# Kernel optimization log

Measured on AMD Instinct MI355X. Metric: run time of the kernel, lower is better.

The kernel has to match this reference:

```python
import jax, jax.numpy as jnp
import numpy as np

TOP_K = 8
ROUTE_SCALE = 2.5
NUM_EXPERTS = 64


def setup_inputs() -> dict:
    key = jax.random.key(0)
    k1, k2, k3 = jax.random.split(key, 3)
    x = jax.random.normal(k1, (16384, 4096), dtype=jnp.float32)
    gate_weight = jax.random.normal(k2, (NUM_EXPERTS, 4096), dtype=jnp.float32) * 0.02
    expert_bias = jax.random.normal(k3, (NUM_EXPERTS,), dtype=jnp.float32) * 0.01
    return {"x": x, "gate_weight": gate_weight, "expert_bias": expert_bias}


def reference(x, gate_weight, expert_bias):
    # gate linear: [T, dim] @ [dim, E] -> [T, E]
    logits = jnp.einsum("td,ed->te", x, gate_weight)
    scores = jax.nn.sigmoid(logits.astype(jnp.float32))  # score_func == 'sigmoid'
    # expert_bias branch: top-k over biased scores, gather unbiased scores
    _, selected_experts_indices = jax.lax.top_k(scores + expert_bias[None, :], TOP_K)
    top_scores = jnp.take_along_axis(scores, selected_experts_indices, axis=1)
    # route_norm (sigmoid normalization)
    denom = top_scores.sum(axis=-1, keepdims=True) + 1e-20
    top_scores = top_scores / denom * ROUTE_SCALE
    # histogram over selected expert indices (torch.histc returns float)
    flat_idx = selected_experts_indices.reshape(-1)
    num_tokens_per_expert = jnp.zeros((NUM_EXPERTS,), jnp.float32).at[flat_idx].add(1.0)
    return top_scores, selected_experts_indices, num_tokens_per_expert
```

## Files before the change

kernel.cpp:

```cpp
#include <hip/hip_runtime.h>
#include <math.h>

#define NTOK 16384
#define DIM  4096
#define NE   64
#define TOPK 8
#define SPLITK 8
#define NSLICE (DIM / SPLITK / 32)
#define ROUTE_SCALE 2.5f

typedef __attribute__((ext_vector_type(8))) short short8v;
typedef __attribute__((ext_vector_type(4))) float f32x4;

__device__ __forceinline__ void split3_pack(const float* v, uint4& b0, uint4& b1, uint4& b2)
{
    uint p0[8], p1[8], p2[8];
#pragma unroll
    for (int j = 0; j < 8; ++j) {
        const float xv = v[j];
        const uint  u0 = __float_as_uint(xv) & 0xffff0000u;
        const float f0 = __uint_as_float(u0);
        const float r  = xv - f0;
        const uint  u1 = __float_as_uint(r) & 0xffff0000u;
        const float f1 = __uint_as_float(u1);
        const float r2 = r - f1;
        const uint  u2 = __float_as_uint(r2) & 0xffff0000u;
        p0[j] = u0; p1[j] = u1; p2[j] = u2;
    }
    b0 = make_uint4(p0[1] | (p0[0] >> 16), p0[3] | (p0[2] >> 16),
                    p0[5] | (p0[4] >> 16), p0[7] | (p0[6] >> 16));
    b1 = make_uint4(p1[1] | (p1[0] >> 16), p1[3] | (p1[2] >> 16),
                    p1[5] | (p1[4] >> 16), p1[7] | (p1[6] >> 16));
    b2 = make_uint4(p2[1] | (p2[0] >> 16), p2[3] | (p2[2] >> 16),
                    p2[5] | (p2[4] >> 16), p2[7] | (p2[6] >> 16));
}

__global__ __launch_bounds__(256)
void prep_w(const float* __restrict__ gw, uint4* __restrict__ wS)
{
    const int tid  = blockIdx.x * 256 + threadIdx.x;
    const int lane = tid & 63;
    const int nt   = (tid >> 6) & 3;
    const int ks   = tid >> 8;
    const int e    = nt * 16 + (lane & 15);
    const int kb   = ks * 32 + (lane >> 4) * 8;
    float v[8];
    *(float4*)&v[0] = *(const float4*)&gw[(size_t)e * DIM + kb];
    *(float4*)&v[4] = *(const float4*)&gw[(size_t)e * DIM + kb + 4];
    uint4 b0, b1, b2;
    split3_pack(v, b0, b1, b2);
    const size_t base = (size_t)(ks * 4 + nt) * 3 * 64 + lane;
    wS[base] = b0; wS[base + 64] = b1; wS[base + 128] = b2;
}

__global__ __launch_bounds__(512, 2)
void router_fused(const float* __restrict__ x, const uint4* __restrict__ wS,
                  const float* __restrict__ bias, float* __restrict__ out)
{
    __shared__ float part_lds[SPLITK][64][NE];
    __shared__ int   hist[NE];

    const int t    = threadIdx.x;
    const int lane = t & 63;
    const int wv   = __builtin_amdgcn_readfirstlane(t >> 6);
    const int r    = lane & 15;
    const int g    = lane >> 4;
    const int tok0 = blockIdx.x * 64;
    const int ks0  = wv * NSLICE;

    if (t < NE) hist[t] = 0;

    const float* xr[4];
#pragma unroll
    for (int G = 0; G < 4; ++G)
        xr[G] = x + (size_t)(tok0 + G * 16 + r) * DIM + ks0 * 32 + g * 8;
    const uint4* wB = wS + lane;

    f32x4 acc[16];
#pragma unroll
    for (int i = 0; i < 16; ++i) acc[i] = (f32x4){0.f, 0.f, 0.f, 0.f};

    float xP[32], xQ[32];
    uint4 bP[12], bQ[12];

#define LOADX(X, s) do {                                                     \
        _Pragma("unroll")                                                    \
        for (int G = 0; G < 4; ++G) {                                        \
            *(float4*)&X[G * 8]     = *(const float4*)(xr[G] + (size_t)(s) * 32);     \
            *(float4*)&X[G * 8 + 4] = *(const float4*)(xr[G] + (size_t)(s) * 32 + 4); \
        }                                                                    \
    } while (0)
#define LOADB(B, s) do {                                                     \
        _Pragma("unroll")                                                    \
        for (int i = 0; i < 12; ++i)                                         \
            B[i] = wB[((size_t)(ks0 + (s)) * 12 + i) * 64];                  \
    } while (0)
#define COMPUTE(X, B) do {                                                            \
        _Pragma("unroll")                                                             \
        for (int G = 0; G < 4; ++G) {                                                 \
            uint4 a0u, a1u, a2u;                                                      \
            split3_pack(&X[G * 8], a0u, a1u, a2u);                                    \
            const short8v a0 = *(short8v*)&a0u;                                       \
            const short8v a1 = *(short8v*)&a1u;                                       \
            const short8v a2 = *(short8v*)&a2u;                                       \
            _Pragma("unroll")                                                         \
            for (int nt = 0; nt < 4; ++nt) {                                          \
                const short8v b0 = *(const short8v*)&B[nt * 3 + 0];                   \
                const short8v b1 = *(const short8v*)&B[nt * 3 + 1];                   \
                const short8v b2 = *(const short8v*)&B[nt * 3 + 2];                   \
                f32x4 c = acc[nt * 4 + G];                                            \
                c = __builtin_amdgcn_mfma_f32_16x16x32_bf16(a2, b0, c, 0, 0, 0);      \
                c = __builtin_amdgcn_mfma_f32_16x16x32_bf16(a1, b1, c, 0, 0, 0);      \
                c = __builtin_amdgcn_mfma_f32_16x16x32_bf16(a0, b2, c, 0, 0, 0);      \
                c = __builtin_amdgcn_mfma_f32_16x16x32_bf16(a1, b0, c, 0, 0, 0);      \
                c = __builtin_amdgcn_mfma_f32_16x16x32_bf16(a0, b1, c, 0, 0, 0);      \
                c = __builtin_amdgcn_mfma_f32_16x16x32_bf16(a0, b0, c, 0, 0, 0);      \
                acc[nt * 4 + G] = c;                                                  \
            }                                                                         \
        }                                                                             \
    } while (0)

    LOADX(xP, 0);
    for (int it = 0; it < NSLICE / 2; ++it) {
        const int s = 2 * it;
        LOADB(bP, s);
        LOADX(xQ, s + 1);
        COMPUTE(xP, bP);
        LOADB(bQ, s + 1);
        const int s2 = (s + 2) & (NSLICE - 1);
        LOADX(xP, s2);
        COMPUTE(xQ, bQ);
    }
#undef LOADX
#undef LOADB
#undef COMPUTE

#pragma unroll
    for (int nt = 0; nt < 4; ++nt)
#pragma unroll
        for (int G = 0; G < 4; ++G)
#pragma unroll
            for (int q = 0; q < 4; ++q)
                part_lds[wv][G * 16 + g * 4 + q][nt * 16 + r] = acc[nt * 4 + G][q];

    __syncthreads();

    const float bias_l = bias[lane];
#pragma unroll 1
    for (int i = 0; i < 8; ++i) {
        const int tok = wv * 8 + i;
        float logit = 0.f;
#pragma unroll
        for (int kh = 0; kh < SPLITK; ++kh)
            logit += part_lds[kh][tok][lane];
        const float s = 1.f / (1.f + expf(-logit));
        float myv  = s + bias_l;
        float outv = 0.f;
        int   outi = 0;
        float sum  = 0.f;
#pragma unroll
        for (int k = 0; k < TOPK; ++k) {
            float cv = myv;
            int   ci = lane;
#pragma unroll
            for (int off = 32; off; off >>= 1) {
                float ov = __shfl_xor(cv, off, 64);
                int   oi = __shfl_xor(ci, off, 64);
                if (ov > cv || (ov == cv && oi < ci)) { cv = ov; ci = oi; }
            }
            float ts = __shfl(s, ci, 64);
            sum += ts;
            if (lane == k)  { outv = ts; outi = ci; }
            if (lane == ci) { myv = -1e30f; }
        }
        const float denom = sum + 1e-20f;
        const size_t gt = (size_t)tok0 + tok;
        if (lane < TOPK) {
            out[gt * TOPK + lane] = (outv / denom) * ROUTE_SCALE;
            out[(size_t)NTOK * TOPK + gt * TOPK + lane] = (float)outi;
            atomicAdd(&hist[outi], 1);
        }
    }

    __syncthreads();
    if (t < NE) {
        int c = hist[t];
        if (c) atomicAdd(&out[(size_t)NTOK * TOPK * 2 + t], (float)c);
    }
}

extern "C" void kernel_launch(void* const* d_in, const int* in_sizes, int n_in,
                              void* d_out, int out_size, void* d_ws, size_t ws_size,
                              hipStream_t stream)
{
    const float* x    = (const float*)d_in[0];
    const float* gw   = (const float*)d_in[1];
    const float* bias = (const float*)d_in[2];
    float* out = (float*)d_out;
    uint4* wS  = (uint4*)d_ws;

    hipMemsetAsync(out + (size_t)NTOK * TOPK * 2, 0, NE * sizeof(float), stream);

    prep_w<<<128, 256, 0, stream>>>(gw, wS);
    router_fused<<<NTOK / 64, 512, 0, stream>>>(x, wS, bias, out);
}
```

Measured before the change: 116.2 us.

## Stage x chunks through swizzled LDS and split waves by token/expert instead of split-K

```diff
diff --git a/kernel.cpp b/kernel.cpp
--- a/kernel.cpp
+++ b/kernel.cpp
@@ -5,8 +5,9 @@
 #define DIM  4096
 #define NE   64
 #define TOPK 8
-#define SPLITK 8
-#define NSLICE (DIM / SPLITK / 32)
+#define CHUNK 256
+#define NCH  (DIM / CHUNK)
+#define SLC  (CHUNK / 32)
 #define ROUTE_SCALE 2.5f
 
 typedef __attribute__((ext_vector_type(8))) short short8v;
@@ -57,103 +58,105 @@
 void router_fused(const float* __restrict__ x, const uint4* __restrict__ wS,
                   const float* __restrict__ bias, float* __restrict__ out)
 {
-    __shared__ float part_lds[SPLITK][64][NE];
+    __shared__ float xs[2][64][CHUNK];
+    __shared__ float sc[64][NE + 1];
     __shared__ int   hist[NE];
 
     const int t    = threadIdx.x;
     const int lane = t & 63;
     const int wv   = __builtin_amdgcn_readfirstlane(t >> 6);
-    const int r    = lane & 15;
+    const int r15  = lane & 15;
     const int g    = lane >> 4;
+    const int tg   = wv & 3;
+    const int eh   = wv >> 2;
     const int tok0 = blockIdx.x * 64;
-    const int ks0  = wv * NSLICE;
 
     if (t < NE) hist[t] = 0;
 
-    const float* xr[4];
-#pragma unroll
-    for (int G = 0; G < 4; ++G)
-        xr[G] = x + (size_t)(tok0 + G * 16 + r) * DIM + ks0 * 32 + g * 8;
-    const uint4* wB = wS + lane;
-
-    f32x4 acc[16];
-#pragma unroll
-    for (int i = 0; i < 16; ++i) acc[i] = (f32x4){0.f, 0.f, 0.f, 0.f};
-
-    float xP[32], xQ[32];
-    uint4 bP[12], bQ[12];
-
-#define LOADX(X, s) do {                                                     \
-        _Pragma("unroll")                                                    \
-        for (int G = 0; G < 4; ++G) {                                        \
-            *(float4*)&X[G * 8]     = *(const float4*)(xr[G] + (size_t)(s) * 32);     \
-            *(float4*)&X[G * 8 + 4] = *(const float4*)(xr[G] + (size_t)(s) * 32 + 4); \
-        }                                                                    \
-    } while (0)
-#define LOADB(B, s) do {                                                     \
-        _Pragma("unroll")                                                    \
-        for (int i = 0; i < 12; ++i)                                         \
-            B[i] = wB[((size_t)(ks0 + (s)) * 12 + i) * 64];                  \
-    } while (0)
-#define COMPUTE(X, B) do {                                                            \
-        _Pragma("unroll")                                                             \
-        for (int G = 0; G < 4; ++G) {                                                 \
-            uint4 a0u, a1u, a2u;                                                      \
-            split3_pack(&X[G * 8], a0u, a1u, a2u);                                    \
-            const short8v a0 = *(short8v*)&a0u;                                       \
-            const short8v a1 = *(short8v*)&a1u;                                       \
-            const short8v a2 = *(short8v*)&a2u;                                       \
-            _Pragma("unroll")                                                         \
-            for (int nt = 0; nt < 4; ++nt) {                                          \
-                const short8v b0 = *(const short8v*)&B[nt * 3 + 0];                   \
-                const short8v b1 = *(const short8v*)&B[nt * 3 + 1];                   \
-                const short8v b2 = *(const short8v*)&B[nt * 3 + 2];                   \
-                f32x4 c = acc[nt * 4 + G];                                            \
-                c = __builtin_amdgcn_mfma_f32_16x16x32_bf16(a2, b0, c, 0, 0, 0);      \
-                c = __builtin_amdgcn_mfma_f32_16x16x32_bf16(a1, b1, c, 0, 0, 0);      \
-                c = __builtin_amdgcn_mfma_f32_16x16x32_bf16(a0, b2, c, 0, 0, 0);      \
-                c = __builtin_amdgcn_mfma_f32_16x16x32_bf16(a1, b0, c, 0, 0, 0);      \
-                c = __builtin_amdgcn_mfma_f32_16x16x32_bf16(a0, b1, c, 0, 0, 0);      \
-                c = __builtin_amdgcn_mfma_f32_16x16x32_bf16(a0, b0, c, 0, 0, 0);      \
-                acc[nt * 4 + G] = c;                                                  \
-            }                                                                         \
-        }                                                                             \
-    } while (0)
-
-    LOADX(xP, 0);
-    for (int it = 0; it < NSLICE / 2; ++it) {
-        const int s = 2 * it;
-        LOADB(bP, s);
-        LOADX(xQ, s + 1);
-        COMPUTE(xP, bP);
-        LOADB(bQ, s + 1);
-        const int s2 = (s + 2) & (NSLICE - 1);
-        LOADX(xP, s2);
-        COMPUTE(xQ, bQ);
-    }
-#undef LOADX
-#undef LOADB
-#undef COMPUTE
-
-#pragma unroll
-    for (int nt = 0; nt < 4; ++nt)
-#pragma unroll
-        for (int G = 0; G < 4; ++G)
-#pragma unroll
-            for (int q = 0; q < 4; ++q)
-                part_lds[wv][G * 16 + g * 4 + q][nt * 16 + r] = acc[nt * 4 + G][q];
-
+    const int row = tg * 16 + r15;
+    const int sw  = r15 & 7;
+    const float* xstage = x + (size_t)(tok0 + wv * 8) * DIM + lane * 4;
+    const uint4* wB = wS + (size_t)(eh * 6) * 64 + lane;
+
+    f32x4 acc[2];
+    acc[0] = (f32x4){0.f, 0.f, 0.f, 0.f};
+    acc[1] = (f32x4){0.f, 0.f, 0.f, 0.f};
+
+    float4 st[8];
+    uint4  b[4][6];
+
+#pragma unroll
+    for (int i = 0; i < 8; ++i)
+        st[i] = *(const float4*)(xstage + (size_t)i * DIM);
+#pragma unroll
+    for (int i = 0; i < 8; ++i)
+        *(float4*)&xs[0][wv * 8 + i][(lane ^ i) * 4] = st[i];
+
+    for (int c = 0; c < NCH; ++c) {
+        const int  cb   = c & 1;
+        const bool more = (c + 1 < NCH);
+        __syncthreads();
+#pragma unroll
+        for (int s = 0; s < 4; ++s)
+#pragma unroll
+            for (int j = 0; j < 6; ++j)
+                b[s][j] = wB[((size_t)(c * SLC + s) * 12 + j) * 64];
+        if (more) {
+#pragma unroll
+            for (int i = 0; i < 8; ++i)
+                st[i] = *(const float4*)(xstage + (size_t)i * DIM + (size_t)(c + 1) * CHUNK);
+        }
+#pragma unroll
+        for (int s = 0; s < SLC; ++s) {
+            float a8[8];
+            const int G0 = s * 8 + g * 2;
+            *(float4*)&a8[0] = *(const float4*)&xs[cb][row][(G0 ^ sw) * 4];
+            *(float4*)&a8[4] = *(const float4*)&xs[cb][row][((G0 + 1) ^ sw) * 4];
+            uint4 a0u, a1u, a2u;
+            split3_pack(a8, a0u, a1u, a2u);
+            const short8v a0 = *(short8v*)&a0u;
+            const short8v a1 = *(short8v*)&a1u;
+            const short8v a2 = *(short8v*)&a2u;
+#pragma unroll
+            for (int ntl = 0; ntl < 2; ++ntl) {
+                const short8v b0 = *(const short8v*)&b[s & 3][ntl * 3 + 0];
+                const short8v b1 = *(const short8v*)&b[s & 3][ntl * 3 + 1];
+                const short8v b2 = *(const short8v*)&b[s & 3][ntl * 3 + 2];
+                f32x4 cc = acc[ntl];
+                cc = __builtin_amdgcn_mfma_f32_16x16x32_bf16(a2, b0, cc, 0, 0, 0);
+                cc = __builtin_amdgcn_mfma_f32_16x16x32_bf16(a1, b1, cc, 0, 0, 0);
+                cc = __builtin_amdgcn_mfma_f32_16x16x32_bf16(a0, b2, cc, 0, 0, 0);
+                cc = __builtin_amdgcn_mfma_f32_16x16x32_bf16(a1, b0, cc, 0, 0, 0);
+                cc = __builtin_amdgcn_mfma_f32_16x16x32_bf16(a0, b1, cc, 0, 0, 0);
+                cc = __builtin_amdgcn_mfma_f32_16x16x32_bf16(a0, b0, cc, 0, 0, 0);
+                acc[ntl] = cc;
+            }
+            if (s < 4) {
+#pragma unroll
+                for (int j = 0; j < 6; ++j)
+                    b[s & 3][j] = wB[((size_t)(c * SLC + s + 4) * 12 + j) * 64];
+            }
+            if (s == 5 && more) {
+#pragma unroll
+                for (int i = 0; i < 8; ++i)
+                    *(float4*)&xs[cb ^ 1][wv * 8 + i][(lane ^ i) * 4] = st[i];
+            }
+        }
+    }
+
+#pragma unroll
+    for (int ntl = 0; ntl < 2; ++ntl)
+#pragma unroll
+        for (int q = 0; q < 4; ++q)
+            sc[tg * 16 + g * 4 + q][eh * 32 + ntl * 16 + r15] =
+                1.f / (1.f + expf(-acc[ntl][q]));
     __syncthreads();
 
     const float bias_l = bias[lane];
 #pragma unroll 1
     for (int i = 0; i < 8; ++i) {
         const int tok = wv * 8 + i;
-        float logit = 0.f;
-#pragma unroll
-        for (int kh = 0; kh < SPLITK; ++kh)
-            logit += part_lds[kh][tok][lane];
-        const float s = 1.f / (1.f + expf(-logit));
+        const float s = sc[tok][lane];
         float myv  = s + bias_l;
         float outv = 0.f;
         int   outi = 0;
@@ -184,8 +187,8 @@
 
     __syncthreads();
     if (t < NE) {
-        int c = hist[t];
-        if (c) atomicAdd(&out[(size_t)NTOK * TOPK * 2 + t], (float)c);
+        int cgt = hist[t];
+        if (cgt) atomicAdd(&out[(size_t)NTOK * TOPK * 2 + t], (float)cgt);
     }
 }
 
```

After: 205.0 us. 1.76x slower.

## Split experts across waves with LDS-staged pre-split x chunks instead of split-K

Applied to the files above, without the earlier changes.

```diff
diff --git a/kernel.cpp b/kernel.cpp
--- a/kernel.cpp
+++ b/kernel.cpp
@@ -5,8 +5,9 @@
 #define DIM  4096
 #define NE   64
 #define TOPK 8
-#define SPLITK 8
-#define NSLICE (DIM / SPLITK / 32)
+#define TPB  32
+#define CHUNK 128
+#define NCH  (DIM / CHUNK)
 #define ROUTE_SCALE 2.5f
 
 typedef __attribute__((ext_vector_type(8))) short short8v;
@@ -33,6 +34,27 @@
                     p1[5] | (p1[4] >> 16), p1[7] | (p1[6] >> 16));
     b2 = make_uint4(p2[1] | (p2[0] >> 16), p2[3] | (p2[2] >> 16),
                     p2[5] | (p2[4] >> 16), p2[7] | (p2[6] >> 16));
+}
+
+__device__ __forceinline__ void split3_pack4(const float4 v, uint2& q0, uint2& q1, uint2& q2)
+{
+    const float vv[4] = {v.x, v.y, v.z, v.w};
+    uint p0[4], p1[4], p2[4];
+#pragma unroll
+    for (int j = 0; j < 4; ++j) {
+        const float xv = vv[j];
+        const uint  u0 = __float_as_uint(xv) & 0xffff0000u;
+        const float f0 = __uint_as_float(u0);
+        const float r  = xv - f0;
+        const uint  u1 = __float_as_uint(r) & 0xffff0000u;
+        const float f1 = __uint_as_float(u1);
+        const float r2 = r - f1;
+        const uint  u2 = __float_as_uint(r2) & 0xffff0000u;
+        p0[j] = u0; p1[j] = u1; p2[j] = u2;
+    }
+    q0 = make_uint2(p0[1] | (p0[0] >> 16), p0[3] | (p0[2] >> 16));
+    q1 = make_uint2(p1[1] | (p1[0] >> 16), p1[3] | (p1[2] >> 16));
+    q2 = make_uint2(p2[1] | (p2[0] >> 16), p2[3] | (p2[2] >> 16));
 }
 
 __global__ __launch_bounds__(256)
@@ -53,107 +75,122 @@
     wS[base] = b0; wS[base + 64] = b1; wS[base + 128] = b2;
 }
 
-__global__ __launch_bounds__(512, 2)
+#define MFMA6(A0, A1, A2, B0, B1, B2, ACC) do {                              \
+    ACC = __builtin_amdgcn_mfma_f32_16x16x32_bf16(A2, B0, ACC, 0, 0, 0);     \
+    ACC = __builtin_amdgcn_mfma_f32_16x16x32_bf16(A1, B1, ACC, 0, 0, 0);     \
+    ACC = __builtin_amdgcn_mfma_f32_16x16x32_bf16(A0, B2, ACC, 0, 0, 0);     \
+    ACC = __builtin_amdgcn_mfma_f32_16x16x32_bf16(A1, B0, ACC, 0, 0, 0);     \
+    ACC = __builtin_amdgcn_mfma_f32_16x16x32_bf16(A0, B1, ACC, 0, 0, 0);     \
+    ACC = __builtin_amdgcn_mfma_f32_16x16x32_bf16(A0, B0, ACC, 0, 0, 0);     \
+} while (0)
+
+__global__ __launch_bounds__(256, 2)
 void router_fused(const float* __restrict__ x, const uint4* __restrict__ wS,
                   const float* __restrict__ bias, float* __restrict__ out)
 {
-    __shared__ float part_lds[SPLITK][64][NE];
-    __shared__ int   hist[NE];
+    __shared__ ushort xp[2][3][TPB][CHUNK];
+    __shared__ float  sc[TPB][NE + 1];
+    __shared__ int    hist[NE];
 
     const int t    = threadIdx.x;
     const int lane = t & 63;
     const int wv   = __builtin_amdgcn_readfirstlane(t >> 6);
-    const int r    = lane & 15;
+    const int r15  = lane & 15;
     const int g    = lane >> 4;
-    const int tok0 = blockIdx.x * 64;
-    const int ks0  = wv * NSLICE;
+    const int tok0 = blockIdx.x * TPB;
 
     if (t < NE) hist[t] = 0;
 
-    const float* xr[4];
-#pragma unroll
-    for (int G = 0; G < 4; ++G)
-        xr[G] = x + (size_t)(tok0 + G * 16 + r) * DIM + ks0 * 32 + g * 8;
-    const uint4* wB = wS + lane;
-
-    f32x4 acc[16];
-#pragma unroll
-    for (int i = 0; i < 16; ++i) acc[i] = (f32x4){0.f, 0.f, 0.f, 0.f};
-
-    float xP[32], xQ[32];
-    uint4 bP[12], bQ[12];
-
-#define LOADX(X, s) do {                                                     \
+    const int srow = t >> 3;
+    const int sg   = t & 7;
+    const float* xsrc = x + (size_t)(tok0 + srow) * DIM + sg * 4;
+
+    const uint4* wB = wS + wv * 192 + lane;
+
+    f32x4 acc0 = {0.f, 0.f, 0.f, 0.f};
+    f32x4 acc1 = {0.f, 0.f, 0.f, 0.f};
+    uint4  B0[12], B1[12];
+    float4 stP[4], stQ[4];
+
+#define STAGE_LOAD(ST, c1) do {                                              \
         _Pragma("unroll")                                                    \
-        for (int G = 0; G < 4; ++G) {                                        \
-            *(float4*)&X[G * 8]     = *(const float4*)(xr[G] + (size_t)(s) * 32);     \
-            *(float4*)&X[G * 8 + 4] = *(const float4*)(xr[G] + (size_t)(s) * 32 + 4); \
+        for (int j = 0; j < 4; ++j)                                          \
+            ST[j] = *(const float4*)(xsrc + (size_t)(c1) * CHUNK + j * 32);  \
+    } while (0)
+
+#define STAGE_WRITE(ST, bb) do {                                             \
+        _Pragma("unroll")                                                    \
+        for (int j = 0; j < 4; ++j) {                                        \
+            uint2 q0, q1, q2;                                                \
+            split3_pack4(ST[j], q0, q1, q2);                                 \
+            const int gg  = sg + 8 * j;                                      \
+            const int off = (((gg >> 1) ^ (srow & 15)) << 3) + ((gg & 1) << 2); \
+            *(uint2*)&xp[bb][0][srow][off] = q0;                             \
+            *(uint2*)&xp[bb][1][srow][off] = q1;                             \
+            *(uint2*)&xp[bb][2][srow][off] = q2;                             \
         }                                                                    \
     } while (0)
-#define LOADB(B, s) do {                                                     \
+
+#define LOADB(B, c1) do {                                                    \
         _Pragma("unroll")                                                    \
-        for (int i = 0; i < 12; ++i)                                         \
-            B[i] = wB[((size_t)(ks0 + (s)) * 12 + i) * 64];                  \
-    } while (0)
-#define COMPUTE(X, B) do {                                                            \
-        _Pragma("unroll")                                                             \
-        for (int G = 0; G < 4; ++G) {                                                 \
-            uint4 a0u, a1u, a2u;                                                      \
-            split3_pack(&X[G * 8], a0u, a1u, a2u);                                    \
-            const short8v a0 = *(short8v*)&a0u;                                       \
-            const short8v a1 = *(short8v*)&a1u;                                       \
-            const short8v a2 = *(short8v*)&a2u;                                       \
-            _Pragma("unroll")                                                         \
-            for (int nt = 0; nt < 4; ++nt) {                                          \
-                const short8v b0 = *(const short8v*)&B[nt * 3 + 0];                   \
-                const short8v b1 = *(const short8v*)&B[nt * 3 + 1];                   \
-                const short8v b2 = *(const short8v*)&B[nt * 3 + 2];                   \
-                f32x4 c = acc[nt * 4 + G];                                            \
-                c = __builtin_amdgcn_mfma_f32_16x16x32_bf16(a2, b0, c, 0, 0, 0);      \
-                c = __builtin_amdgcn_mfma_f32_16x16x32_bf16(a1, b1, c, 0, 0, 0);      \
-                c = __builtin_amdgcn_mfma_f32_16x16x32_bf16(a0, b2, c, 0, 0, 0);      \
-                c = __builtin_amdgcn_mfma_f32_16x16x32_bf16(a1, b0, c, 0, 0, 0);      \
-                c = __builtin_amdgcn_mfma_f32_16x16x32_bf16(a0, b1, c, 0, 0, 0);      \
-                c = __builtin_amdgcn_mfma_f32_16x16x32_bf16(a0, b0, c, 0, 0, 0);      \
-                acc[nt * 4 + G] = c;                                                  \
-            }                                                                         \
-        }                                                                             \
-    } while (0)
-
-    LOADX(xP, 0);
-    for (int it = 0; it < NSLICE / 2; ++it) {
-        const int s = 2 * it;
-        LOADB(bP, s);
-        LOADX(xQ, s + 1);
-        COMPUTE(xP, bP);
-        LOADB(bQ, s + 1);
-        const int s2 = (s + 2) & (NSLICE - 1);
-        LOADX(xP, s2);
-        COMPUTE(xQ, bQ);
-    }
-#undef LOADX
+        for (int s2 = 0; s2 < 4; ++s2)                                       \
+            _Pragma("unroll")                                                \
+            for (int sp = 0; sp < 3; ++sp)                                   \
+                B[s2 * 3 + sp] = wB[(size_t)((c1) * 4 + s2) * 768 + sp * 64];\
+    } while (0)
+
+#define SLICE(B, cb, s) do {                                                 \
+        const int off = ((((s) * 4 + g) ^ r15) << 3);                        \
+        const short8v a0_0 = *(const short8v*)&xp[cb][0][r15][off];          \
+        const short8v a1_0 = *(const short8v*)&xp[cb][1][r15][off];          \
+        const short8v a2_0 = *(const short8v*)&xp[cb][2][r15][off];          \
+        const short8v a0_1 = *(const short8v*)&xp[cb][0][16 + r15][off];     \
+        const short8v a1_1 = *(const short8v*)&xp[cb][1][16 + r15][off];     \
+        const short8v a2_1 = *(const short8v*)&xp[cb][2][16 + r15][off];     \
+        const short8v b0 = *(const short8v*)&B[(s) * 3 + 0];                 \
+        const short8v b1 = *(const short8v*)&B[(s) * 3 + 1];                 \
+        const short8v b2 = *(const short8v*)&B[(s) * 3 + 2];                 \
+        MFMA6(a0_0, a1_0, a2_0, b0, b1, b2, acc0);                           \
+        MFMA6(a0_1, a1_1, a2_1, b0, b1, b2, acc1);                           \
+    } while (0)
+
+#define CHUNK_BODY(c, BU, BV, STW, STL) do {                                 \
+        __syncthreads();                                                     \
+        SLICE(BU, (c) & 1, 0);                                               \
+        SLICE(BU, (c) & 1, 1);                                               \
+        SLICE(BU, (c) & 1, 2);                                               \
+        SLICE(BU, (c) & 1, 3);                                               \
+        if ((c) + 1 < NCH) { LOADB(BV, (c) + 1); STAGE_WRITE(STW, ((c) & 1) ^ 1); } \
+        if ((c) + 2 < NCH) { STAGE_LOAD(STL, (c) + 2); }                     \
+    } while (0)
+
+    LOADB(B0, 0);
+    STAGE_LOAD(stP, 0);
+    STAGE_WRITE(stP, 0);
+    STAGE_LOAD(stP, 1);
+
+    for (int c = 0; c < NCH; c += 2) {
+        CHUNK_BODY(c,     B0, B1, stP, stQ);
+        CHUNK_BODY(c + 1, B1, B0, stQ, stP);
+    }
+#undef STAGE_LOAD
+#undef STAGE_WRITE
 #undef LOADB
-#undef COMPUTE
-
-#pragma unroll
-    for (int nt = 0; nt < 4; ++nt)
-#pragma unroll
-        for (int G = 0; G < 4; ++G)
-#pragma unroll
-            for (int q = 0; q < 4; ++q)
-                part_lds[wv][G * 16 + g * 4 + q][nt * 16 + r] = acc[nt * 4 + G][q];
-
+#undef SLICE
+#undef CHUNK_BODY
+
+#pragma unroll
+    for (int q = 0; q < 4; ++q) {
+        sc[g * 4 + q][wv * 16 + r15]      = 1.f / (1.f + expf(-acc0[q]));
+        sc[16 + g * 4 + q][wv * 16 + r15] = 1.f / (1.f + expf(-acc1[q]));
+    }
     __syncthreads();
 
     const float bias_l = bias[lane];
 #pragma unroll 1
     for (int i = 0; i < 8; ++i) {
         const int tok = wv * 8 + i;
-        float logit = 0.f;
-#pragma unroll
-        for (int kh = 0; kh < SPLITK; ++kh)
-            logit += part_lds[kh][tok][lane];
-        const float s = 1.f / (1.f + expf(-logit));
+        const float s = sc[tok][lane];
         float myv  = s + bias_l;
         float outv = 0.f;
         int   outi = 0;
@@ -184,8 +221,8 @@
 
     __syncthreads();
     if (t < NE) {
-        int c = hist[t];
-        if (c) atomicAdd(&out[(size_t)NTOK * TOPK * 2 + t], (float)c);
+        int cgt = hist[t];
+        if (cgt) atomicAdd(&out[(size_t)NTOK * TOPK * 2 + t], (float)cgt);
     }
 }
 
@@ -202,5 +239,5 @@
     hipMemsetAsync(out + (size_t)NTOK * TOPK * 2, 0, NE * sizeof(float), stream);
 
     prep_w<<<128, 256, 0, stream>>>(gw, wS);
-    router_fused<<<NTOK / 64, 512, 0, stream>>>(x, wS, bias, out);
-}
+    router_fused<<<NTOK / TPB, 256, 0, stream>>>(x, wS, bias, out);
+}
```

New measurement: 112.4 us. -3.3%, faster.
